# Kernel optimization log

Hardware: AMD Instinct MI355X
Metric: run time of the kernel (lower is better)

## Reference

```python
import jax, jax.numpy as jnp
import numpy as np

B, F, C, H, W = 16, 256, 64, 64, 64   # batch, features, z_channels(e_dim), height, width
N_E = 512                              # codebooksize
BETA = 1.0
EPS = 1e-5


def setup_inputs() -> dict:
    key = jax.random.key(0)
    ks = jax.random.split(key, 4)
    x = jax.random.normal(ks[0], (B, F, H, W), jnp.float32)
    emb = jax.random.normal(ks[1], (N_E, C), jnp.float32)
    emb = emb / jnp.linalg.norm(emb, axis=1, keepdims=True)  # points on hypersphere
    return dict(
        x=x,
        bn1_gamma=jnp.ones((F,), jnp.float32),
        bn1_beta=jnp.zeros((F,), jnp.float32),
        conv1_w=jax.random.normal(ks[2], (C, F), jnp.float32) * np.float32(1.0 / np.sqrt(F)),
        conv1_b=jnp.zeros((C,), jnp.float32),
        conv2_w=jax.random.normal(ks[3], (C, C), jnp.float32) * np.float32(1.0 / np.sqrt(C)),
        conv2_b=jnp.zeros((C,), jnp.float32),
        embedding=emb,
        r=jnp.ones((N_E,), jnp.float32),
    )


def reference(x, bn1_gamma, bn1_beta, conv1_w, conv1_b, conv2_w, conv2_b, embedding, r):
    sg = jax.lax.stop_gradient
    # BatchNorm2d (training mode: batch stats, biased variance)
    mu = x.mean(axis=(0, 2, 3), keepdims=True)
    var = x.var(axis=(0, 2, 3), keepdims=True)
    x1 = (x - mu) * jax.lax.rsqrt(var + EPS)
    x1 = x1 * bn1_gamma[None, :, None, None] + bn1_beta[None, :, None, None]
    # 1x1 convs (note: original overwrites norm2 output, conv2 consumes conv1 output directly)
    x1 = jnp.einsum('bfhw,cf->bchw', x1, conv1_w) + conv1_b[None, :, None, None]
    z = jnp.einsum('bchw,oc->bohw', x1, conv2_w) + conv2_b[None, :, None, None]

    zf = z.reshape(-1, C)  # [B*C*H*W/e_dim view == flat rows of e_dim]
    # codebook angular statistics (norms detached, as torch.Tensor(list) detaches)
    d1 = embedding @ embedding.T                                 # [n_e, n_e]
    en = sg(jnp.linalg.norm(embedding, axis=1))                  # [n_e]
    edx = jnp.clip(d1 / (en[:, None] * en[None, :]), -0.99999, 0.99999)
    ang = jnp.arccos(edx)
    total_min_distance = jnp.mean(jnp.sort(ang, axis=0)[1])      # kthvalue(.,2,dim=0)
    codebookvariance = jnp.mean(jnp.var(ang, axis=1, ddof=1))    # torch.var unbiased

    # VQ dispatch: squared L2 distances + argmin + gather
    d = (zf ** 2).sum(1, keepdims=True) + (embedding ** 2).sum(1) - 2.0 * (zf @ embedding.T)
    idx = jnp.argmin(d, axis=1)                                  # [ntok]
    z_q = embedding[idx].reshape(z.shape)

    hsw = jnp.mean(jnp.square(r - en))
    # legacy=True path with beta=1.0, ignorezq=False, disentangle=True
    loss = jnp.mean((sg(z_q) - z) ** 2) + BETA * jnp.mean((z_q - sg(z)) ** 2)
    loss = loss + hsw + (codebookvariance - total_min_distance)

    z_q = z + sg(z_q - z)  # straight-through
    cb_loss = jnp.float32(0.0)  # prev_cb is None
    r_c = r + sg(jnp.clip(r, 0.9, 1.1) - r)  # Clamp with straight-through grad
    mean_r = jnp.mean(r_c)
    return (loss, z_q, codebookvariance, total_min_distance, hsw, cb_loss, mean_r)
```

## Files before the change

### kernel.cpp

```cpp
#include <hip/hip_runtime.h>
#include <math.h>


#define CAP    2048
#define MARGIN 4e-3f

#define WS_WHI  0
#define WS_WLO  8192
#define WS_BP   16384
#define WS_EN   16448
#define WS_E2   16960
#define WS_ACC  17472
#define WS_CNT  17480
#define WS_WL   17488
#define WS_EFT  19536
#define WS_WD   52304
#define WS_BPD  85072
#define WS_EHI  85200
#define WS_ELO  101584
#define WS_PART 117968
#define WS_SV   122064
#define WS_SM   122576

typedef __attribute__((ext_vector_type(8))) __bf16 bf16v8;
typedef __attribute__((ext_vector_type(2))) __bf16 bf16v2;
typedef __attribute__((ext_vector_type(4))) float  f32v4;
typedef __attribute__((ext_vector_type(4))) unsigned u32v4;

__device__ __forceinline__ unsigned short f2bf(float f) {
    __bf16 h = (__bf16)f;
    return __builtin_bit_cast(unsigned short, h);
}
__device__ __forceinline__ float bf2f(unsigned short h) {
    union { unsigned u; float f; } v; v.u = ((unsigned)h) << 16; return v.f;
}
__device__ __forceinline__ unsigned pack_bf2(float a, float b) {
    bf16v2 v = { (__bf16)a, (__bf16)b };
    return __builtin_bit_cast(unsigned, v);
}
__device__ __forceinline__ float bfhi(float a) {
    return (float)(__bf16)a;
}
__device__ __forceinline__ void load_lds16(const float* g, unsigned* l) {
    __builtin_amdgcn_global_load_lds((const __attribute__((address_space(1))) void*)g,
                                     (__attribute__((address_space(3))) void*)l, 16, 0, 0);
}

__global__ __launch_bounds__(256) void bn_stats_prep(
    const float* __restrict__ x, double* __restrict__ part,
    const float* __restrict__ emb,
    float* __restrict__ eft, float* __restrict__ en, float* __restrict__ e2,
    unsigned short* __restrict__ ehi, unsigned short* __restrict__ elo,
    float* __restrict__ sv, float* __restrict__ sm)
{
    const int t = threadIdx.x;

    if (blockIdx.x < 1024) {
        const int f = blockIdx.x >> 2, ch = blockIdx.x & 3;
        double s0 = 0.0, s1 = 0.0, q0 = 0.0, q1 = 0.0, q2 = 0.0, q3 = 0.0;
        #pragma unroll
        for (int bb = 0; bb < 4; ++bb) {
            const int b = ch * 4 + bb;
            const float4* p = (const float4*)(x + ((size_t)(b * 256 + f) << 12));
            #pragma unroll
            for (int ii = 0; ii < 4; ++ii) {
                float4 u = p[t + ii * 256];
                double dx = u.x, dy = u.y, dz = u.z, dw = u.w;
                s0 += dx + dy; s1 += dz + dw;
                q0 = fma(dx, dx, q0); q1 = fma(dy, dy, q1);
                q2 = fma(dz, dz, q2); q3 = fma(dw, dw, q3);
            }
        }
        double s = s0 + s1, q = (q0 + q1) + (q2 + q3);
        #pragma unroll
        for (int off = 32; off; off >>= 1) { s += __shfl_xor(s, off, 64); q += __shfl_xor(q, off, 64); }
        __shared__ double sh[8];
        const int wv = t >> 6;
        if ((t & 63) == 0) { sh[wv * 2] = s; sh[wv * 2 + 1] = q; }
        __syncthreads();
        if (t == 0) {
            part[blockIdx.x * 2]     = (sh[0] + sh[2]) + (sh[4] + sh[6]);
            part[blockIdx.x * 2 + 1] = (sh[1] + sh[3]) + (sh[5] + sh[7]);
        }
    } else if (blockIdx.x < 1088) {
        const int blk = blockIdx.x - 1024;
        const int lane = t & 63, wv = t >> 6;
        #pragma unroll
        for (int rr = 0; rr < 2; ++rr) {
            int n = blk * 8 + rr * 4 + wv;
            float v = emb[n * 64 + lane];
            eft[lane * 512 + n] = v;
            unsigned short hb = f2bf(v);
            unsigned short lb = f2bf(v - bf2f(hb));
            int pos = (lane >> 3) ^ (n & 7);
            ehi[n * 64 + pos * 8 + (lane & 7)] = hb;
            elo[n * 64 + pos * 8 + (lane & 7)] = lb;
            float qq = v * v;
            #pragma unroll
            for (int off = 32; off; off >>= 1) qq += __shfl_xor(qq, off, 64);
            if (lane == 0) { e2[n] = qq; en[n] = sqrtf(qq); }
        }
    } else {
        const int i = blockIdx.x - 1088;
        const int lane = t & 63, wv = t >> 6;
        __shared__ float ei_sh[64];
        __shared__ float ang[512];
        if (t < 64) ei_sh[t] = emb[(i << 6) + t];
        __syncthreads();
        float ni0 = 0.f, ni1 = 0.f, ni2 = 0.f, ni3 = 0.f;
        #pragma unroll
        for (int k = 0; k < 64; k += 4) {
            ni0 = fmaf(ei_sh[k + 0], ei_sh[k + 0], ni0);
            ni1 = fmaf(ei_sh[k + 1], ei_sh[k + 1], ni1);
            ni2 = fmaf(ei_sh[k + 2], ei_sh[k + 2], ni2);
            ni3 = fmaf(ei_sh[k + 3], ei_sh[k + 3], ni3);
        }
        const float eni = sqrtf((ni0 + ni1) + (ni2 + ni3));
        #pragma unroll
        for (int jj = 0; jj < 2; ++jj) {
            const int j = t + jj * 256;
            const float4* er = (const float4*)(emb + ((size_t)j << 6));
            float d0 = 0.f, d1 = 0.f, d2 = 0.f, d3 = 0.f;
            float n0 = 0.f, n1 = 0.f, n2 = 0.f, n3 = 0.f;
            #pragma unroll
            for (int k4 = 0; k4 < 16; ++k4) {
                float4 u = er[k4];
                const float* e4 = ei_sh + k4 * 4;
                d0 = fmaf(u.x, e4[0], d0); d1 = fmaf(u.y, e4[1], d1);
                d2 = fmaf(u.z, e4[2], d2); d3 = fmaf(u.w, e4[3], d3);
                n0 = fmaf(u.x, u.x, n0);   n1 = fmaf(u.y, u.y, n1);
                n2 = fmaf(u.z, u.z, n2);   n3 = fmaf(u.w, u.w, n3);
            }
            float dot = (d0 + d1) + (d2 + d3);
            float enj = sqrtf((n0 + n1) + (n2 + n3));
            float xv = dot / (eni * enj);
            xv = fminf(fmaxf(xv, -0.99999f), 0.99999f);
            ang[j] = acosf(xv);
        }
        __syncthreads();
        if (wv == 0) {
            float m1 = 3.4e38f, m2 = 3.4e38f, ssum = 0.f;
            #pragma unroll
            for (int t8 = 0; t8 < 8; ++t8) {
                float a = ang[t8 * 64 + lane];
                ssum += a;
                if (a < m1) { m2 = m1; m1 = a; }
                else if (a < m2) m2 = a;
            }
            #pragma unroll
            for (int off = 32; off; off >>= 1) ssum += __shfl_xor(ssum, off, 64);
            #pragma unroll
            for (int off = 32; off; off >>= 1) {
                float o1 = __shfl_xor(m1, off, 64);
                float o2 = __shfl_xor(m2, off, 64);
                if (o1 < m1) { m2 = fminf(m1, o2); m1 = o1; }
                else          m2 = fminf(m2, o1);
            }
            float mean = ssum * (1.f / 512.f);
            float vs = 0.f;
            #pragma unroll
            for (int t8 = 0; t8 < 8; ++t8) {
                float tt = ang[t8 * 64 + lane] - mean;
                vs = fmaf(tt, tt, vs);
            }
            #pragma unroll
            for (int off = 32; off; off >>= 1) vs += __shfl_xor(vs, off, 64);
            if (lane == 0) { sv[i] = vs * (1.f / 511.f); sm[i] = m2; }
        }
    }
}

__global__ __launch_bounds__(256) void prep(
    const float* __restrict__ w1, const float* __restrict__ w2,
    const float* __restrict__ b1, const float* __restrict__ b2,
    const float* __restrict__ gamma, const float* __restrict__ beta,
    const double* __restrict__ part,
    unsigned short* __restrict__ whi, unsigned short* __restrict__ wlo,
    double* __restrict__ Wd,
    double* __restrict__ bpd, float* __restrict__ bp,
    float* __restrict__ accs, int* __restrict__ cnt)
{
    __shared__ double sh_ad[4];
    __shared__ double cdl[256];
    __shared__ double red[4][64];
    __shared__ double tsh[64];
    const int t = threadIdx.x;

    if (blockIdx.x < 64) {
        const int o = t & 63, fi = t >> 6;
        const int f = blockIdx.x * 4 + fi;
        if (o == 0) {
            double s = (part[(4 * f) * 2]     + part[(4 * f + 1) * 2])
                     + (part[(4 * f + 2) * 2] + part[(4 * f + 3) * 2]);
            double q = (part[(4 * f) * 2 + 1]     + part[(4 * f + 1) * 2 + 1])
                     + (part[(4 * f + 2) * 2 + 1] + part[(4 * f + 3) * 2 + 1]);
            double mean = s * (1.0 / 65536.0);
            double var  = q * (1.0 / 65536.0) - mean * mean;
            sh_ad[fi] = (double)gamma[f] / sqrt(var + 1e-5);
        }
        __syncthreads();
        double s = 0.0;
        for (int c = 0; c < 64; ++c)
            s = fma((double)w2[o * 64 + c], (double)w1[c * 256 + f], s);
        double wp = s * sh_ad[fi];
        Wd[o * 256 + f] = wp;
        {
            float wpf = (float)wp;
            unsigned short wh = f2bf(wpf);
            unsigned short wlv = f2bf(wpf - bf2f(wh));
            int mt = o >> 4, cq_ = o & 15, sK = f >> 5, qd_ = (f >> 3) & 3, j = f & 7;
            int idx = ((mt * 8 + sK) * 64 + qd_ * 16 + cq_) * 8 + j;
            whi[idx] = wh; wlo[idx] = wlv;
        }
    } else {
        {
            const int f = t;
            double s = (part[(4 * f) * 2]     + part[(4 * f + 1) * 2])
                     + (part[(4 * f + 2) * 2] + part[(4 * f + 3) * 2]);
            double q = (part[(4 * f) * 2 + 1]     + part[(4 * f + 1) * 2 + 1])
                     + (part[(4 * f + 2) * 2 + 1] + part[(4 * f + 3) * 2 + 1]);
            double mean = s * (1.0 / 65536.0);
            double var  = q * (1.0 / 65536.0) - mean * mean;
            double a = (double)gamma[f] / sqrt(var + 1e-5);
            cdl[f] = (double)beta[f] - mean * a;
        }
        __syncthreads();
        const int o = t & 63, p = t >> 6;
        double ss = 0.0;
        for (int j = 0; j < 64; ++j) {
            int fidx = p * 64 + j;
            ss = fma((double)w1[o * 256 + fidx], cdl[fidx], ss);
        }
        red[p][o] = ss; __syncthreads();
        if (t < 64) tsh[t] = (double)b1[t] + (red[0][t] + red[1][t]) + (red[2][t] + red[3][t]);
        __syncthreads();
        if (t < 64) {
            double bb = (double)b2[t];
            for (int c = 0; c < 64; ++c)
                bb = fma((double)w2[t * 64 + c], tsh[c], bb);
            bpd[t] = bb;
            bp[t]  = (float)bb;
        }
        if (t < 8) accs[t] = 0.f;
        if (t == 0) cnt[0] = 0;
    }
}

__global__ __launch_bounds__(256, 4) void fused_gemm_vq(
    const float* __restrict__ x,
    const unsigned short* __restrict__ whi,
    const unsigned short* __restrict__ wlo,
    const float* __restrict__ bp,
    const float* __restrict__ emb,
    const float* __restrict__ e2,
    const unsigned short* __restrict__ ehi,
    const unsigned short* __restrict__ elo,
    float* __restrict__ accs,
    int* __restrict__ cnt, int* __restrict__ wl,
    float* __restrict__ zq)
{
    __shared__ __align__(16) unsigned smem[4880];
    enum { OAR = 0,
           OE2 = 4096, OZ2 = 4608, ODT = 4672, OD2T = 4736, OIT = 4800 };
    float* e2s = (float*)(smem + OE2);
    float* z2s = (float*)(smem + OZ2);
    float* dT  = (float*)(smem + ODT);
    float* d2T = (float*)(smem + OD2T);
    int*   iT  = (int*)(smem + OIT);

    const int tid = threadIdx.x, lane = tid & 63, wv = tid >> 6;
    const int wvu = __builtin_amdgcn_readfirstlane(wv);
    const int lb = ((blockIdx.x & 7) << 7) | (blockIdx.x >> 3);
    const int b = lb >> 6, h = lb & 63;
    const int cq = lane & 15, qd = lane >> 4;

    bf16v8 Ahi[8], Alo[8];
    #pragma unroll
    for (int s = 0; s < 8; ++s) {
        Ahi[s] = *(const bf16v8*)(whi + ((size_t)((wvu * 8 + s) * 64 + lane)) * 8);
        Alo[s] = *(const bf16v8*)(wlo + ((size_t)((wvu * 8 + s) * 64 + lane)) * 8);
    }
    float bpv[4];
    #pragma unroll
    for (int r = 0; r < 4; ++r) bpv[r] = bp[wvu * 16 + qd * 4 + r];
    e2s[tid]       = e2[tid];
    e2s[tid + 256] = e2[tid + 256];

    const float* xb = x + ((size_t)(b * 256 + wvu * 16) << 12) + (h << 6) + lane;
    float xva[16], xvb[16];
    #pragma unroll
    for (int i = 0; i < 16; ++i) xva[i] = xb[(size_t)i << 12];
    #pragma unroll
    for (int i = 0; i < 16; ++i) xvb[i] = xb[((size_t)(64 + i)) << 12];

    f32v4 acc[4];
    #pragma unroll
    for (int nt = 0; nt < 4; ++nt) acc[nt] = (f32v4){bpv[0], bpv[1], bpv[2], bpv[3]};

#define GEMM_CHUNK(CHK, CUR)                                                          \
    {                                                                                 \
        __syncthreads();                                                 \
        {                                                                             \
            unsigned hb[8], lbv[8];                                                   \
            _Pragma("unroll")                                                         \
            for (int p = 0; p < 8; ++p) {                                             \
                float a = CUR[2 * p], bq = CUR[2 * p + 1];                            \
                hb[p] = pack_bf2(a, bq);                                              \
                lbv[p] = pack_bf2(a - bfhi(a), bq - bfhi(bq));                        \
            }                                                                         \
            const int b0 = lane * 32 + (((2 * wvu) ^ (lane & 7)) << 2);               \
            const int b1 = lane * 32 + (((2 * wvu + 1) ^ (lane & 7)) << 2);           \
            *(u32v4*)(smem + OAR + b0)        = (u32v4){hb[0], hb[1], hb[2], hb[3]};  \
            *(u32v4*)(smem + OAR + b1)        = (u32v4){hb[4], hb[5], hb[6], hb[7]};  \
            *(u32v4*)(smem + OAR + 2048 + b0) = (u32v4){lbv[0], lbv[1], lbv[2], lbv[3]}; \
            *(u32v4*)(smem + OAR + 2048 + b1) = (u32v4){lbv[4], lbv[5], lbv[6], lbv[7]}; \
        }                                                                             \
        __syncthreads();                                                \
        if (CHK < 2) {                               \
            const float* xb2 = xb + ((size_t)((CHK + 2) * 64) << 12);                 \
            _Pragma("unroll")                                                         \
            for (int i = 0; i < 16; ++i) CUR[i] = xb2[(size_t)i << 12];               \
        }                                                                             \
        _Pragma("unroll")                                                             \
        for (int st2 = 0; st2 < 2; ++st2) {                                           \
            const int s = CHK * 2 + st2;                                              \
            _Pragma("unroll")                                                         \
            for (int nt = 0; nt < 4; ++nt) {                                          \
                const int row = nt * 16 + cq;                                         \
                const int pos = row * 32 + (((st2 * 4 + qd) ^ (row & 7)) << 2);       \
                bf16v8 bh = *(const bf16v8*)(smem + OAR + pos);                       \
                bf16v8 bl = *(const bf16v8*)(smem + OAR + 2048 + pos);                \
                acc[nt] = __builtin_amdgcn_mfma_f32_16x16x32_bf16(Ahi[s], bh, acc[nt], 0, 0, 0); \
                acc[nt] = __builtin_amdgcn_mfma_f32_16x16x32_bf16(Ahi[s], bl, acc[nt], 0, 0, 0); \
                acc[nt] = __builtin_amdgcn_mfma_f32_16x16x32_bf16(Alo[s], bh, acc[nt], 0, 0, 0); \
            }                                                                         \
        }                                                                             \
    }

    GEMM_CHUNK(0, xva)
    GEMM_CHUNK(1, xvb)
    GEMM_CHUNK(2, xva)
    GEMM_CHUNK(3, xvb)
#undef GEMM_CHUNK

    __syncthreads();

    {
        float z2p[4];
        #pragma unroll
        for (int r = 0; r < 4; ++r) {
            float p2 = 0.f;
            #pragma unroll
            for (int nt = 0; nt < 4; ++nt) p2 = fmaf(acc[nt][r], acc[nt][r], p2);
            #pragma unroll
            for (int off = 1; off <= 8; off <<= 1) p2 += __shfl_xor(p2, off, 64);
            z2p[r] = p2;
        }
        if (cq == 0) {
            #pragma unroll
            for (int r = 0; r < 4; ++r) z2s[wvu * 16 + qd * 4 + r] = z2p[r];
        }
        unsigned short* ar = (unsigned short*)(smem + OAR);
        #pragma unroll
        for (int nt = 0; nt < 4; ++nt) {
            const int w = nt * 16 + cq;
            const int gz = w >> 3, kj = w & 7;
            #pragma unroll
            for (int r = 0; r < 4; ++r) {
                const int tok = wvu * 16 + qd * 4 + r;
                const int hw = tok * 64 + ((gz ^ (tok & 7)) << 3) + kj;
                unsigned short zh = f2bf(acc[nt][r]);
                ar[hw]        = zh;
                ar[4096 + hw] = f2bf(acc[nt][r] - bf2f(zh));
            }
        }
    }
    __syncthreads();

    const int x7 = cq & 7;
    bf16v8 vahi[2], valo[2];
    {
        const int rbase = (wvu * 16 + cq) * 32;
        #pragma unroll
        for (int s = 0; s < 2; ++s) {
            int pos = ((s * 4 + qd) ^ x7) * 4;
            vahi[s] = *(const bf16v8*)(smem + OAR + rbase + pos);
            valo[s] = *(const bf16v8*)(smem + OAR + 2048 + rbase + pos);
        }
    }
    __syncthreads();

    {
        const float* gh = (const float*)ehi;
        const float* gl = (const float*)elo;
        load_lds16(gh + wvu * 256 + lane * 4,        smem + OAR + wvu * 256);
        load_lds16(gl + wvu * 256 + lane * 4,        smem + OAR + 1024 + wvu * 256);
        load_lds16(gh + 1024 + wvu * 256 + lane * 4, smem + OAR + 2048 + wvu * 256);
        load_lds16(gl + 1024 + wvu * 256 + lane * 4, smem + OAR + 3072 + wvu * 256);
    }

    float m1[4] = {-3.4e38f, -3.4e38f, -3.4e38f, -3.4e38f};
    float m2[4] = {-3.4e38f, -3.4e38f, -3.4e38f, -3.4e38f};
    int   i1[4] = {0, 0, 0, 0};
    const int p0 = (qd ^ x7) * 4, p1 = ((4 + qd) ^ x7) * 4;

    #pragma unroll 1
    for (int t2 = 0; t2 < 32; ++t2) {
        if ((t2 & 1) == 0) {
            __syncthreads();
            int st = t2 >> 1;
            if (st >= 1 && st < 15) {
                const float* gh = (const float*)ehi + (size_t)(st + 1) * 1024;
                const float* gl = (const float*)elo + (size_t)(st + 1) * 1024;
                unsigned* dst = smem + OAR + ((st + 1) & 1) * 2048;
                load_lds16(gh + wvu * 256 + lane * 4, dst + wvu * 256);
                load_lds16(gl + wvu * 256 + lane * 4, dst + 1024 + wvu * 256);
            }
        }
        const int rb = OAR + ((t2 >> 1) & 1) * 2048 + ((t2 & 1) * 16 + cq) * 32;
        bf16v8 bh0 = *(const bf16v8*)(smem + rb + p0);
        bf16v8 bh1 = *(const bf16v8*)(smem + rb + p1);
        bf16v8 bl0 = *(const bf16v8*)(smem + rb + 1024 + p0);
        bf16v8 bl1 = *(const bf16v8*)(smem + rb + 1024 + p1);
        const float eps = e2s[t2 * 16 + cq];
        f32v4 a = {0.f, 0.f, 0.f, 0.f};
        __builtin_amdgcn_s_setprio(1);
        a = __builtin_amdgcn_mfma_f32_16x16x32_bf16(vahi[0], bh0, a, 0, 0, 0);
        a = __builtin_amdgcn_mfma_f32_16x16x32_bf16(vahi[1], bh1, a, 0, 0, 0);
        a = __builtin_amdgcn_mfma_f32_16x16x32_bf16(vahi[0], bl0, a, 0, 0, 0);
        a = __builtin_amdgcn_mfma_f32_16x16x32_bf16(vahi[1], bl1, a, 0, 0, 0);
        a = __builtin_amdgcn_mfma_f32_16x16x32_bf16(valo[0], bh0, a, 0, 0, 0);
        a = __builtin_amdgcn_mfma_f32_16x16x32_bf16(valo[1], bh1, a, 0, 0, 0);
        __builtin_amdgcn_s_setprio(0);
        const int n = t2 * 16 + cq;
        #pragma unroll
        for (int r = 0; r < 4; ++r) {
            float s = fmaf(-0.5f, eps, a[r]);
            bool gt = s > m1[r];
            m2[r] = fminf(fmaxf(s, m2[r]), m1[r]);
            i1[r] = gt ? n : i1[r];
            m1[r] = fmaxf(s, m1[r]);
        }
    }

    #pragma unroll
    for (int r = 0; r < 4; ++r) {
        #pragma unroll
        for (int off = 1; off <= 8; off <<= 1) {
            float o1 = __shfl_xor(m1[r], off, 64);
            float o2 = __shfl_xor(m2[r], off, 64);
            int   oi = __shfl_xor(i1[r], off, 64);
            if (o1 > m1[r] || (o1 == m1[r] && oi < i1[r])) {
                m2[r] = fmaxf(m1[r], o2); m1[r] = o1; i1[r] = oi;
            } else {
                m2[r] = fmaxf(m2[r], o1);
            }
        }
    }
    if (cq == 0) {
        #pragma unroll
        for (int r = 0; r < 4; ++r) {
            int tok = wvu * 16 + qd * 4 + r;
            dT[tok] = m1[r]; d2T[tok] = m2[r]; iT[tok] = i1[r];
        }
    }
    __syncthreads();

    if (wv == 0) {
        float s1 = dT[lane], s2 = d2T[lane];
        if (s1 - s2 < MARGIN * 0.5f) {
            int pos = atomicAdd(cnt, 1);
            if (pos < CAP) wl[pos] = ((b << 6) + lane) * 64 + h;
        }
        float ms = z2s[lane] - 2.f * s1;
        #pragma unroll
        for (int off = 32; off; off >>= 1) ms += __shfl_xor(ms, off, 64);
        if (lane == 0) atomicAdd(accs + 0, ms);
    }
    __syncthreads();

    float* zrow = zq + ((size_t)(b * 64) << 12) + (h << 6) + lane;
    #pragma unroll
    for (int cc = 0; cc < 16; ++cc) {
        int c = wvu * 16 + cc;
        int id = iT[c];
        zrow[(size_t)c << 12] = emb[(id << 6) + lane];
    }
}

__global__ __launch_bounds__(256) void refine_fin(
    const float* __restrict__ x,
    const double* __restrict__ Wd,
    const double* __restrict__ bpd,
    const float* __restrict__ emb,
    const float* __restrict__ eft,
    const int* __restrict__ cnt, const int* __restrict__ wl,
    float* __restrict__ zq,
    const float* __restrict__ accs, const float* __restrict__ en,
    const float* __restrict__ sv, const float* __restrict__ sm,
    const float* __restrict__ r, float* __restrict__ out)
{
    const int tid = threadIdx.x, lane = tid & 63, wv = tid >> 6;

    if (blockIdx.x == 2048) {
        if (wv == 0) {
            float hs = 0.f, rs = 0.f, cv = 0.f, tm = 0.f;
            #pragma unroll
            for (int jj = 0; jj < 8; ++jj) {
                int n = (jj << 6) + lane;
                float rv = r[n];
                float d = rv - en[n];
                hs = fmaf(d, d, hs);
                rs += fminf(fmaxf(rv, 0.9f), 1.1f);
                cv += sv[n];
                tm += sm[n];
            }
            #pragma unroll
            for (int off = 32; off; off >>= 1) {
                hs += __shfl_xor(hs, off, 64); rs += __shfl_xor(rs, off, 64);
                cv += __shfl_xor(cv, off, 64); tm += __shfl_xor(tm, off, 64);
            }
            if (lane == 0) {
                float hsw    = hs * (1.f / 512.f);
                float mean_r = rs * (1.f / 512.f);
                float mse    = accs[0] * (1.f / 4194304.f);
                float cbv    = cv * (1.f / 512.f);
                float tmd    = tm * (1.f / 512.f);
                float loss   = 2.f * mse + hsw + (cbv - tmd);
                out[0]       = loss;
                out[4194305] = cbv;
                out[4194306] = tmd;
                out[4194307] = hsw;
                out[4194308] = 0.f;
                out[4194309] = mean_r;
            }
        }
        return;
    }

    int count = cnt[0]; if (count > CAP) count = CAP;
    const int it = blockIdx.x;
    if (it >= count) return;

    __shared__ double zp[4][64];
    __shared__ double zs[64];
    __shared__ double dsh[4];
    __shared__ int    ish[4];

    const int r2 = wl[it];
    const int b = r2 >> 12, c = (r2 >> 6) & 63, h = r2 & 63;

    {
        const float* xp = x + (((size_t)(b * 256 + wv * 64)) << 12) + (h << 6) + lane;
        const double* wrow = Wd + c * 256 + wv * 64;
        double zc0 = 0.0, zc1 = 0.0, zc2 = 0.0, zc3 = 0.0;
        double zc4 = 0.0, zc5 = 0.0, zc6 = 0.0, zc7 = 0.0;
        #pragma unroll
        for (int f = 0; f < 64; f += 8) {
            float a0 = xp[(size_t)(f + 0) << 12];
            float a1 = xp[(size_t)(f + 1) << 12];
            float a2 = xp[(size_t)(f + 2) << 12];
            float a3 = xp[(size_t)(f + 3) << 12];
            float a4 = xp[(size_t)(f + 4) << 12];
            float a5 = xp[(size_t)(f + 5) << 12];
            float a6 = xp[(size_t)(f + 6) << 12];
            float a7 = xp[(size_t)(f + 7) << 12];
            zc0 = fma(wrow[f + 0], (double)a0, zc0);
            zc1 = fma(wrow[f + 1], (double)a1, zc1);
            zc2 = fma(wrow[f + 2], (double)a2, zc2);
            zc3 = fma(wrow[f + 3], (double)a3, zc3);
            zc4 = fma(wrow[f + 4], (double)a4, zc4);
            zc5 = fma(wrow[f + 5], (double)a5, zc5);
            zc6 = fma(wrow[f + 6], (double)a6, zc6);
            zc7 = fma(wrow[f + 7], (double)a7, zc7);
        }
        zp[wv][lane] = ((zc0 + zc1) + (zc2 + zc3)) + ((zc4 + zc5) + (zc6 + zc7));
    }
    __syncthreads();
    if (tid < 64) zs[tid] = (zp[0][tid] + zp[1][tid]) + (zp[2][tid] + zp[3][tid]) + bpd[c];
    __syncthreads();

    const int n0 = tid, n1 = tid + 256;
    double d0a = 0.0, d0b = 0.0, d0c = 0.0, d0d = 0.0;
    double d1a = 0.0, d1b = 0.0, d1c = 0.0, d1d = 0.0;
    #pragma unroll 4
    for (int k = 0; k < 64; k += 4) {
        double z0 = zs[k], z1 = zs[k + 1], z2 = zs[k + 2], z3 = zs[k + 3];
        double t;
        t = z0 - (double)eft[((k + 0) << 9) + n0]; d0a = fma(t, t, d0a);
        t = z1 - (double)eft[((k + 1) << 9) + n0]; d0b = fma(t, t, d0b);
        t = z2 - (double)eft[((k + 2) << 9) + n0]; d0c = fma(t, t, d0c);
        t = z3 - (double)eft[((k + 3) << 9) + n0]; d0d = fma(t, t, d0d);
        t = z0 - (double)eft[((k + 0) << 9) + n1]; d1a = fma(t, t, d1a);
        t = z1 - (double)eft[((k + 1) << 9) + n1]; d1b = fma(t, t, d1b);
        t = z2 - (double)eft[((k + 2) << 9) + n1]; d1c = fma(t, t, d1c);
        t = z3 - (double)eft[((k + 3) << 9) + n1]; d1d = fma(t, t, d1d);
    }
    double d0 = (d0a + d0b) + (d0c + d0d);
    double d1 = (d1a + d1b) + (d1c + d1d);
    double dm; int im;
    if (d1 < d0) { dm = d1; im = n1; } else { dm = d0; im = n0; }

    #pragma unroll
    for (int off = 32; off; off >>= 1) {
        double od = __shfl_xor(dm, off, 64);
        int    oi = __shfl_xor(im, off, 64);
        if (od < dm || (od == dm && oi < im)) { dm = od; im = oi; }
    }
    if (lane == 0) { dsh[wv] = dm; ish[wv] = im; }
    __syncthreads();

    if (tid < 64) {
        double best = dsh[0]; int bi = ish[0];
        #pragma unroll
        for (int wq = 1; wq < 4; ++wq) {
            double od = dsh[wq]; int oi = ish[wq];
            if (od < best || (od == best && oi < bi)) { best = od; bi = oi; }
        }
        zq[((size_t)r2 << 6) + tid] = emb[(bi << 6) + tid];
    }
}

extern "C" void kernel_launch(void* const* d_in, const int* in_sizes, int n_in,
                              void* d_out, int out_size, void* d_ws, size_t ws_size,
                              hipStream_t stream) {
    const float* x   = (const float*)d_in[0];
    const float* g1  = (const float*)d_in[1];
    const float* be1 = (const float*)d_in[2];
    const float* w1  = (const float*)d_in[3];
    const float* b1  = (const float*)d_in[4];
    const float* w2  = (const float*)d_in[5];
    const float* b2  = (const float*)d_in[6];
    const float* emb = (const float*)d_in[7];
    const float* r   = (const float*)d_in[8];
    float* ws = (float*)d_ws;
    float* out = (float*)d_out;

    double* WD   = (double*)(ws + WS_WD);
    double* BPD  = (double*)(ws + WS_BPD);
    double* PART = (double*)(ws + WS_PART);
    int*    CNT  = (int*)(ws + WS_CNT);
    int*    WL   = (int*)(ws + WS_WL);
    unsigned short* WHI = (unsigned short*)(ws + WS_WHI);
    unsigned short* WLO = (unsigned short*)(ws + WS_WLO);
    unsigned short* EHI = (unsigned short*)(ws + WS_EHI);
    unsigned short* ELO = (unsigned short*)(ws + WS_ELO);

    bn_stats_prep<<<1600, 256, 0, stream>>>(x, PART, emb,
                                            ws + WS_EFT, ws + WS_EN, ws + WS_E2,
                                            EHI, ELO, ws + WS_SV, ws + WS_SM);
    prep<<<65, 256, 0, stream>>>(w1, w2, b1, b2, g1, be1, PART,
                                 WHI, WLO, WD, BPD, ws + WS_BP,
                                 ws + WS_ACC, CNT);
    fused_gemm_vq<<<1024, 256, 0, stream>>>(x, WHI, WLO, ws + WS_BP,
                                            emb, ws + WS_E2,
                                            EHI, ELO, ws + WS_ACC, CNT, WL, out + 1);
    refine_fin<<<2049, 256, 0, stream>>>(x, WD, BPD, emb, ws + WS_EFT, CNT, WL,
                                         out + 1, ws + WS_ACC, ws + WS_EN,
                                         ws + WS_SV, ws + WS_SM, r, out);
}
```

Baseline: 181.7 us.

## Eliminate prep kernel by folding BN scale into GEMM consumers

Removes the separate prep launch. The unscaled W2·W1 product and its bf16 hi/lo split are now computed inside the stats kernel, which does not depend on x. Each fused_gemm_vq block recomputes the BN scale/shift and folded bias from the partial sums, then applies the per-feature scale to x before the bf16 split. refine_fin likewise recomputes scale and bias per block, and accumulator zeroing moves to a memset. This saves one launch and its serialization, at the cost of redundant per-block prologue work (256-way reductions and 64x64 double dot products) in 1024 and 2049 blocks. The hi/lo bf16 split now covers the unscaled weights and separately the scaled activations, which shifts rounding error.

Measured after the change: 190.7 us. 4.9% more time.

```diff
diff --git a/kernel.cpp b/kernel.cpp
--- a/kernel.cpp
+++ b/kernel.cpp
@@ -7,7 +7,6 @@
 
 #define WS_WHI  0
 #define WS_WLO  8192
-#define WS_BP   16384
 #define WS_EN   16448
 #define WS_E2   16960
 #define WS_ACC  17472
@@ -15,7 +14,6 @@
 #define WS_WL   17488
 #define WS_EFT  19536
 #define WS_WD   52304
-#define WS_BPD  85072
 #define WS_EHI  85200
 #define WS_ELO  101584
 #define WS_PART 117968
@@ -46,44 +44,87 @@
                                      (__attribute__((address_space(3))) void*)l, 16, 0, 0);
 }
 
-__global__ __launch_bounds__(256) void bn_stats_prep(
+__global__ __launch_bounds__(256) void bn_stats_fold(
     const float* __restrict__ x, double* __restrict__ part,
     const float* __restrict__ emb,
+    const float* __restrict__ w1, const float* __restrict__ w2,
     float* __restrict__ eft, float* __restrict__ en, float* __restrict__ e2,
     unsigned short* __restrict__ ehi, unsigned short* __restrict__ elo,
-    float* __restrict__ sv, float* __restrict__ sm)
+    float* __restrict__ sv, float* __restrict__ sm,
+    double* __restrict__ Ud,
+    unsigned short* __restrict__ whi, unsigned short* __restrict__ wlo)
 {
     const int t = threadIdx.x;
 
-    if (blockIdx.x < 1024) {
-        const int f = blockIdx.x >> 2, ch = blockIdx.x & 3;
-        double s0 = 0.0, s1 = 0.0, q0 = 0.0, q1 = 0.0, q2 = 0.0, q3 = 0.0;
-        #pragma unroll
-        for (int bb = 0; bb < 4; ++bb) {
-            const int b = ch * 4 + bb;
-            const float4* p = (const float4*)(x + ((size_t)(b * 256 + f) << 12));
-            #pragma unroll
-            for (int ii = 0; ii < 4; ++ii) {
-                float4 u = p[t + ii * 256];
-                double dx = u.x, dy = u.y, dz = u.z, dw = u.w;
-                s0 += dx + dy; s1 += dz + dw;
-                q0 = fma(dx, dx, q0); q1 = fma(dy, dy, q1);
-                q2 = fma(dz, dz, q2); q3 = fma(dw, dw, q3);
-            }
-        }
-        double s = s0 + s1, q = (q0 + q1) + (q2 + q3);
-        #pragma unroll
-        for (int off = 32; off; off >>= 1) { s += __shfl_xor(s, off, 64); q += __shfl_xor(q, off, 64); }
-        __shared__ double sh[8];
-        const int wv = t >> 6;
-        if ((t & 63) == 0) { sh[wv * 2] = s; sh[wv * 2 + 1] = q; }
+    if (blockIdx.x < 512) {
+        const int i = blockIdx.x;
+        const int lane = t & 63, wv = t >> 6;
+        __shared__ float ei_sh[64];
+        __shared__ float ang[512];
+        if (t < 64) ei_sh[t] = emb[(i << 6) + t];
         __syncthreads();
-        if (t == 0) {
-            part[blockIdx.x * 2]     = (sh[0] + sh[2]) + (sh[4] + sh[6]);
-            part[blockIdx.x * 2 + 1] = (sh[1] + sh[3]) + (sh[5] + sh[7]);
-        }
-    } else if (blockIdx.x < 1088) {
-        const int blk = blockIdx.x - 1024;
+        float ni0 = 0.f, ni1 = 0.f, ni2 = 0.f, ni3 = 0.f;
+        #pragma unroll
+        for (int k = 0; k < 64; k += 4) {
+            ni0 = fmaf(ei_sh[k + 0], ei_sh[k + 0], ni0);
+            ni1 = fmaf(ei_sh[k + 1], ei_sh[k + 1], ni1);
+            ni2 = fmaf(ei_sh[k + 2], ei_sh[k + 2], ni2);
+            ni3 = fmaf(ei_sh[k + 3], ei_sh[k + 3], ni3);
+        }
+        const float eni = sqrtf((ni0 + ni1) + (ni2 + ni3));
+        #pragma unroll
+        for (int jj = 0; jj < 2; ++jj) {
+            const int j = t + jj * 256;
+            const float4* er = (const float4*)(emb + ((size_t)j << 6));
+            float d0 = 0.f, d1 = 0.f, d2 = 0.f, d3 = 0.f;
+            float n0 = 0.f, n1 = 0.f, n2 = 0.f, n3 = 0.f;
+            #pragma unroll
+            for (int k4 = 0; k4 < 16; ++k4) {
+                float4 u = er[k4];
+                const float* e4 = ei_sh + k4 * 4;
+                d0 = fmaf(u.x, e4[0], d0); d1 = fmaf(u.y, e4[1], d1);
+                d2 = fmaf(u.z, e4[2], d2); d3 = fmaf(u.w, e4[3], d3);
+                n0 = fmaf(u.x, u.x, n0);   n1 = fmaf(u.y, u.y, n1);
+                n2 = fmaf(u.z, u.z, n2);   n3 = fmaf(u.w, u.w, n3);
+            }
+            float dot = (d0 + d1) + (d2 + d3);
+            float enj = sqrtf((n0 + n1) + (n2 + n3));
+            float xv = dot / (eni * enj);
+            xv = fminf(fmaxf(xv, -0.99999f), 0.99999f);
+            ang[j] = acosf(xv);
+        }
+        __syncthreads();
+        if (wv == 0) {
+            float m1 = 3.4e38f, m2 = 3.4e38f, ssum = 0.f;
+            #pragma unroll
+            for (int t8 = 0; t8 < 8; ++t8) {
+                float a = ang[t8 * 64 + lane];
+                ssum += a;
+                if (a < m1) { m2 = m1; m1 = a; }
+                else if (a < m2) m2 = a;
+            }
+            #pragma unroll
+            for (int off = 32; off; off >>= 1) ssum += __shfl_xor(ssum, off, 64);
+            #pragma unroll
+            for (int off = 32; off; off >>= 1) {
+                float o1 = __shfl_xor(m1, off, 64);
+                float o2 = __shfl_xor(m2, off, 64);
+                if (o1 < m1) { m2 = fminf(m1, o2); m1 = o1; }
+                else          m2 = fminf(m2, o1);
+            }
+            float mean = ssum * (1.f / 512.f);
+            float vs = 0.f;
+            #pragma unroll
+            for (int t8 = 0; t8 < 8; ++t8) {
+                float tt = ang[t8 * 64 + lane] - mean;
+                vs = fmaf(tt, tt, vs);
+            }
+            #pragma unroll
+            for (int off = 32; off; off >>= 1) vs += __shfl_xor(vs, off, 64);
+            if (lane == 0) { sv[i] = vs * (1.f / 511.f); sm[i] = m2; }
+        }
+    } else if (blockIdx.x < 576) {
+        const int blk = blockIdx.x - 512;
         const int lane = t & 63, wv = t >> 6;
         #pragma unroll
         for (int rr = 0; rr < 2; ++rr) {
@@ -100,149 +141,48 @@
             for (int off = 32; off; off >>= 1) qq += __shfl_xor(qq, off, 64);
             if (lane == 0) { e2[n] = qq; en[n] = sqrtf(qq); }
         }
-    } else {
-        const int i = blockIdx.x - 1088;
-        const int lane = t & 63, wv = t >> 6;
-        __shared__ float ei_sh[64];
-        __shared__ float ang[512];
-        if (t < 64) ei_sh[t] = emb[(i << 6) + t];
-        __syncthreads();
-        float ni0 = 0.f, ni1 = 0.f, ni2 = 0.f, ni3 = 0.f;
-        #pragma unroll
-        for (int k = 0; k < 64; k += 4) {
-            ni0 = fmaf(ei_sh[k + 0], ei_sh[k + 0], ni0);
-            ni1 = fmaf(ei_sh[k + 1], ei_sh[k + 1], ni1);
-            ni2 = fmaf(ei_sh[k + 2], ei_sh[k + 2], ni2);
-            ni3 = fmaf(ei_sh[k + 3], ei_sh[k + 3], ni3);
-        }
-        const float eni = sqrtf((ni0 + ni1) + (ni2 + ni3));
-        #pragma unroll
-        for (int jj = 0; jj < 2; ++jj) {
-            const int j = t + jj * 256;
-            const float4* er = (const float4*)(emb + ((size_t)j << 6));
-            float d0 = 0.f, d1 = 0.f, d2 = 0.f, d3 = 0.f;
-            float n0 = 0.f, n1 = 0.f, n2 = 0.f, n3 = 0.f;
-            #pragma unroll
-            for (int k4 = 0; k4 < 16; ++k4) {
-                float4 u = er[k4];
-                const float* e4 = ei_sh + k4 * 4;
-                d0 = fmaf(u.x, e4[0], d0); d1 = fmaf(u.y, e4[1], d1);
-                d2 = fmaf(u.z, e4[2], d2); d3 = fmaf(u.w, e4[3], d3);
-                n0 = fmaf(u.x, u.x, n0);   n1 = fmaf(u.y, u.y, n1);
-                n2 = fmaf(u.z, u.z, n2);   n3 = fmaf(u.w, u.w, n3);
-            }
-            float dot = (d0 + d1) + (d2 + d3);
-            float enj = sqrtf((n0 + n1) + (n2 + n3));
-            float xv = dot / (eni * enj);
-            xv = fminf(fmaxf(xv, -0.99999f), 0.99999f);
-            ang[j] = acosf(xv);
-        }
-        __syncthreads();
-        if (wv == 0) {
-            float m1 = 3.4e38f, m2 = 3.4e38f, ssum = 0.f;
-            #pragma unroll
-            for (int t8 = 0; t8 < 8; ++t8) {
-                float a = ang[t8 * 64 + lane];
-                ssum += a;
-                if (a < m1) { m2 = m1; m1 = a; }
-                else if (a < m2) m2 = a;
-            }
-            #pragma unroll
-            for (int off = 32; off; off >>= 1) ssum += __shfl_xor(ssum, off, 64);
-            #pragma unroll
-            for (int off = 32; off; off >>= 1) {
-                float o1 = __shfl_xor(m1, off, 64);
-                float o2 = __shfl_xor(m2, off, 64);
-                if (o1 < m1) { m2 = fminf(m1, o2); m1 = o1; }
-                else          m2 = fminf(m2, o1);
-            }
-            float mean = ssum * (1.f / 512.f);
-            float vs = 0.f;
-            #pragma unroll
-            for (int t8 = 0; t8 < 8; ++t8) {
-                float tt = ang[t8 * 64 + lane] - mean;
-                vs = fmaf(tt, tt, vs);
-            }
-            #pragma unroll
-            for (int off = 32; off; off >>= 1) vs += __shfl_xor(vs, off, 64);
-            if (lane == 0) { sv[i] = vs * (1.f / 511.f); sm[i] = m2; }
-        }
-    }
-}
-
-__global__ __launch_bounds__(256) void prep(
-    const float* __restrict__ w1, const float* __restrict__ w2,
-    const float* __restrict__ b1, const float* __restrict__ b2,
-    const float* __restrict__ gamma, const float* __restrict__ beta,
-    const double* __restrict__ part,
-    unsigned short* __restrict__ whi, unsigned short* __restrict__ wlo,
-    double* __restrict__ Wd,
-    double* __restrict__ bpd, float* __restrict__ bp,
-    float* __restrict__ accs, int* __restrict__ cnt)
-{
-    __shared__ double sh_ad[4];
-    __shared__ double cdl[256];
-    __shared__ double red[4][64];
-    __shared__ double tsh[64];
-    const int t = threadIdx.x;
-
-    if (blockIdx.x < 64) {
+    } else if (blockIdx.x < 640) {
+        const int blk = blockIdx.x - 576;
         const int o = t & 63, fi = t >> 6;
-        const int f = blockIdx.x * 4 + fi;
-        if (o == 0) {
-            double s = (part[(4 * f) * 2]     + part[(4 * f + 1) * 2])
-                     + (part[(4 * f + 2) * 2] + part[(4 * f + 3) * 2]);
-            double q = (part[(4 * f) * 2 + 1]     + part[(4 * f + 1) * 2 + 1])
-                     + (part[(4 * f + 2) * 2 + 1] + part[(4 * f + 3) * 2 + 1]);
-            double mean = s * (1.0 / 65536.0);
-            double var  = q * (1.0 / 65536.0) - mean * mean;
-            sh_ad[fi] = (double)gamma[f] / sqrt(var + 1e-5);
-        }
-        __syncthreads();
+        const int f = blk * 4 + fi;
         double s = 0.0;
         for (int c = 0; c < 64; ++c)
             s = fma((double)w2[o * 64 + c], (double)w1[c * 256 + f], s);
-        double wp = s * sh_ad[fi];
-        Wd[o * 256 + f] = wp;
-        {
-            float wpf = (float)wp;
-            unsigned short wh = f2bf(wpf);
-            unsigned short wlv = f2bf(wpf - bf2f(wh));
-            int mt = o >> 4, cq_ = o & 15, sK = f >> 5, qd_ = (f >> 3) & 3, j = f & 7;
-            int idx = ((mt * 8 + sK) * 64 + qd_ * 16 + cq_) * 8 + j;
-            whi[idx] = wh; wlo[idx] = wlv;
-        }
+        Ud[o * 256 + f] = s;
+        float wpf = (float)s;
+        unsigned short wh = f2bf(wpf);
+        unsigned short wlv = f2bf(wpf - bf2f(wh));
+        int mt = o >> 4, cq_ = o & 15, sK = f >> 5, qd_ = (f >> 3) & 3, j = f & 7;
+        int idx = ((mt * 8 + sK) * 64 + qd_ * 16 + cq_) * 8 + j;
+        whi[idx] = wh; wlo[idx] = wlv;
     } else {
-        {
-            const int f = t;
-            double s = (part[(4 * f) * 2]     + part[(4 * f + 1) * 2])
-                     + (part[(4 * f + 2) * 2] + part[(4 * f + 3) * 2]);
-            double q = (part[(4 * f) * 2 + 1]     + part[(4 * f + 1) * 2 + 1])
-                     + (part[(4 * f + 2) * 2 + 1] + part[(4 * f + 3) * 2 + 1]);
-            double mean = s * (1.0 / 65536.0);
-            double var  = q * (1.0 / 65536.0) - mean * mean;
-            double a = (double)gamma[f] / sqrt(var + 1e-5);
-            cdl[f] = (double)beta[f] - mean * a;
-        }
+        const int idx = blockIdx.x - 640;
+        const int f = idx >> 2, ch = idx & 3;
+        double s0 = 0.0, s1 = 0.0, q0 = 0.0, q1 = 0.0, q2 = 0.0, q3 = 0.0;
+        #pragma unroll
+        for (int bb = 0; bb < 4; ++bb) {
+            const int b = ch * 4 + bb;
+            const float4* p = (const float4*)(x + ((size_t)(b * 256 + f) << 12));
+            #pragma unroll
+            for (int ii = 0; ii < 4; ++ii) {
+                float4 u = p[t + ii * 256];
+                double dx = u.x, dy = u.y, dz = u.z, dw = u.w;
+                s0 += dx + dy; s1 += dz + dw;
+                q0 = fma(dx, dx, q0); q1 = fma(dy, dy, q1);
+                q2 = fma(dz, dz, q2); q3 = fma(dw, dw, q3);
+            }
+        }
+        double s = s0 + s1, q = (q0 + q1) + (q2 + q3);
+        #pragma unroll
+        for (int off = 32; off; off >>= 1) { s += __shfl_xor(s, off, 64); q += __shfl_xor(q, off, 64); }
+        __shared__ double sh[8];
+        const int wv = t >> 6;
+        if ((t & 63) == 0) { sh[wv * 2] = s; sh[wv * 2 + 1] = q; }
         __syncthreads();
-        const int o = t & 63, p = t >> 6;
-        double ss = 0.0;
-        for (int j = 0; j < 64; ++j) {
-            int fidx = p * 64 + j;
-            ss = fma((double)w1[o * 256 + fidx], cdl[fidx], ss);
-        }
-        red[p][o] = ss; __syncthreads();
-        if (t < 64) tsh[t] = (double)b1[t] + (red[0][t] + red[1][t]) + (red[2][t] + red[3][t]);
-        __syncthreads();
-        if (t < 64) {
-            double bb = (double)b2[t];
-            for (int c = 0; c < 64; ++c)
-                bb = fma((double)w2[t * 64 + c], tsh[c], bb);
-            bpd[t] = bb;
-            bp[t]  = (float)bb;
-        }
-        if (t < 8) accs[t] = 0.f;
-        if (t == 0) cnt[0] = 0;
+        if (t == 0) {
+            part[idx * 2]     = (sh[0] + sh[2]) + (sh[4] + sh[6]);
+            part[idx * 2 + 1] = (sh[1] + sh[3]) + (sh[5] + sh[7]);
+        }
     }
 }
 
@@ -250,7 +190,10 @@
     const float* __restrict__ x,
     const unsigned short* __restrict__ whi,
     const unsigned short* __restrict__ wlo,
-    const float* __restrict__ bp,
+    const double* __restrict__ part,
+    const float* __restrict__ gamma, const float* __restrict__ beta,
+    const float* __restrict__ w1, const float* __restrict__ b1,
+    const float* __restrict__ w2, const float* __restrict__ b2,
     const float* __restrict__ emb,
     const float* __restrict__ e2,
     const unsigned short* __restrict__ ehi,
@@ -274,17 +217,54 @@
     const int b = lb >> 6, h = lb & 63;
     const int cq = lane & 15, qd = lane >> 4;
 
+    float bpv[4];
+    {
+        double* cdl  = (double*)(smem + OAR);
+        double* red  = (double*)(smem + OAR + 512);
+        double* tshd = (double*)(smem + OAR + 1024);
+        float*  bpf  = (float*)(smem + OAR + 1152);
+        float*  af_s = (float*)(smem + OE2);
+        {
+            const int f = tid;
+            double s = (part[(4 * f) * 2]     + part[(4 * f + 1) * 2])
+                     + (part[(4 * f + 2) * 2] + part[(4 * f + 3) * 2]);
+            double q = (part[(4 * f) * 2 + 1]     + part[(4 * f + 1) * 2 + 1])
+                     + (part[(4 * f + 2) * 2 + 1] + part[(4 * f + 3) * 2 + 1]);
+            double mean = s * (1.0 / 65536.0);
+            double var  = q * (1.0 / 65536.0) - mean * mean;
+            double a = (double)gamma[f] / sqrt(var + 1e-5);
+            af_s[f] = (float)a;
+            cdl[f]  = (double)beta[f] - mean * a;
+        }
+        __syncthreads();
+        {
+            const int o = tid & 63, p = tid >> 6;
+            double ss = 0.0;
+            for (int j = 0; j < 64; ++j)
+                ss = fma((double)w1[o * 256 + p * 64 + j], cdl[p * 64 + j], ss);
+            red[p * 64 + o] = ss;
+        }
+        __syncthreads();
+        if (tid < 64) tshd[tid] = (double)b1[tid] + (red[tid] + red[64 + tid]) + (red[128 + tid] + red[192 + tid]);
+        __syncthreads();
+        if (tid < 64) {
+            double bb = (double)b2[tid];
+            for (int k = 0; k < 64; ++k)
+                bb = fma((double)w2[tid * 64 + k], tshd[k], bb);
+            bpf[tid] = (float)bb;
+        }
+        __syncthreads();
+        #pragma unroll
+        for (int r = 0; r < 4; ++r) bpv[r] = bpf[wvu * 16 + qd * 4 + r];
+    }
+    const float* af_s = (const float*)(smem + OE2);
+
     bf16v8 Ahi[8], Alo[8];
     #pragma unroll
     for (int s = 0; s < 8; ++s) {
         Ahi[s] = *(const bf16v8*)(whi + ((size_t)((wvu * 8 + s) * 64 + lane)) * 8);
         Alo[s] = *(const bf16v8*)(wlo + ((size_t)((wvu * 8 + s) * 64 + lane)) * 8);
     }
-    float bpv[4];
-    #pragma unroll
-    for (int r = 0; r < 4; ++r) bpv[r] = bp[wvu * 16 + qd * 4 + r];
-    e2s[tid]       = e2[tid];
-    e2s[tid + 256] = e2[tid + 256];
 
     const float* xb = x + ((size_t)(b * 256 + wvu * 16) << 12) + (h << 6) + lane;
     float xva[16], xvb[16];
@@ -299,21 +279,25 @@
 
 #define GEMM_CHUNK(CHK, CUR)                                                          \
     {                                                                                 \
+        float afv[16];                                                                \
+        _Pragma("unroll")                                                             \
+        for (int i = 0; i < 16; ++i) afv[i] = af_s[CHK * 64 + wvu * 16 + i];          \
         __syncthreads();                                                 \
         {                                                                             \
             unsigned hb[8], lbv[8];                                                   \
             _Pragma("unroll")                                                         \
             for (int p = 0; p < 8; ++p) {                                             \
-                float a = CUR[2 * p], bq = CUR[2 * p + 1];                            \
+                float a = afv[2 * p] * CUR[2 * p];                                    \
+                float bq = afv[2 * p + 1] * CUR[2 * p + 1];                           \
                 hb[p] = pack_bf2(a, bq);                                              \
                 lbv[p] = pack_bf2(a - bfhi(a), bq - bfhi(bq));                        \
             }                                                                         \
             const int b0 = lane * 32 + (((2 * wvu) ^ (lane & 7)) << 2);               \
-            const int b1 = lane * 32 + (((2 * wvu + 1) ^ (lane & 7)) << 2);           \
-            *(u32v4*)(smem + OAR + b0)        = (u32v4){hb[0], hb[1], hb[2], hb[3]};  \
-            *(u32v4*)(smem + OAR + b1)        = (u32v4){hb[4], hb[5], hb[6], hb[7]};  \
-            *(u32v4*)(smem + OAR + 2048 + b0) = (u32v4){lbv[0], lbv[1], lbv[2], lbv[3]}; \
-            *(u32v4*)(smem + OAR + 2048 + b1) = (u32v4){lbv[4], lbv[5], lbv[6], lbv[7]}; \
+            const int b1_ = lane * 32 + (((2 * wvu + 1) ^ (lane & 7)) << 2);          \
+            *(u32v4*)(smem + OAR + b0)         = (u32v4){hb[0], hb[1], hb[2], hb[3]}; \
+            *(u32v4*)(smem + OAR + b1_)        = (u32v4){hb[4], hb[5], hb[6], hb[7]}; \
+            *(u32v4*)(smem + OAR + 2048 + b0)  = (u32v4){lbv[0], lbv[1], lbv[2], lbv[3]}; \
+            *(u32v4*)(smem + OAR + 2048 + b1_) = (u32v4){lbv[4], lbv[5], lbv[6], lbv[7]}; \
         }                                                                             \
         __syncthreads();                                                \
         if (CHK < 2) {                               \
@@ -345,6 +329,9 @@
 
     __syncthreads();
 
+    e2s[tid]       = e2[tid];
+    e2s[tid + 256] = e2[tid + 256];
+
     {
         float z2p[4];
         #pragma unroll
@@ -490,8 +477,11 @@
 
 __global__ __launch_bounds__(256) void refine_fin(
     const float* __restrict__ x,
-    const double* __restrict__ Wd,
-    const double* __restrict__ bpd,
+    const double* __restrict__ Ud,
+    const double* __restrict__ part,
+    const float* __restrict__ gamma, const float* __restrict__ beta,
+    const float* __restrict__ b1, const float* __restrict__ b2,
+    const float* __restrict__ w2,
     const float* __restrict__ emb,
     const float* __restrict__ eft,
     const int* __restrict__ cnt, const int* __restrict__ wl,
@@ -546,13 +536,36 @@
     __shared__ double zs[64];
     __shared__ double dsh[4];
     __shared__ int    ish[4];
+    __shared__ double adl[256];
+    __shared__ double bsh;
 
     const int r2 = wl[it];
     const int b = r2 >> 12, c = (r2 >> 6) & 63, h = r2 & 63;
 
     {
+        const int f = tid;
+        double s = (part[(4 * f) * 2]     + part[(4 * f + 1) * 2])
+                 + (part[(4 * f + 2) * 2] + part[(4 * f + 3) * 2]);
+        double q = (part[(4 * f) * 2 + 1]     + part[(4 * f + 1) * 2 + 1])
+                 + (part[(4 * f + 2) * 2 + 1] + part[(4 * f + 3) * 2 + 1]);
+        double mean = s * (1.0 / 65536.0);
+        double var  = q * (1.0 / 65536.0) - mean * mean;
+        double a = (double)gamma[f] / sqrt(var + 1e-5);
+        adl[f] = a;
+        double cdlv = (double)beta[f] - mean * a;
+        double p = Ud[c * 256 + f] * cdlv;
+        if (tid < 64) p = fma((double)w2[c * 64 + tid], (double)b1[tid], p);
+        #pragma unroll
+        for (int off = 32; off; off >>= 1) p += __shfl_xor(p, off, 64);
+        if (lane == 0) dsh[wv] = p;
+    }
+    __syncthreads();
+    if (tid == 0) bsh = (double)b2[c] + (dsh[0] + dsh[1]) + (dsh[2] + dsh[3]);
+
+    {
         const float* xp = x + (((size_t)(b * 256 + wv * 64)) << 12) + (h << 6) + lane;
-        const double* wrow = Wd + c * 256 + wv * 64;
+        const double* urow = Ud + c * 256 + wv * 64;
+        const double* arow = adl + wv * 64;
         double zc0 = 0.0, zc1 = 0.0, zc2 = 0.0, zc3 = 0.0;
         double zc4 = 0.0, zc5 = 0.0, zc6 = 0.0, zc7 = 0.0;
         #pragma unroll
@@ -565,19 +578,19 @@
             float a5 = xp[(size_t)(f + 5) << 12];
             float a6 = xp[(size_t)(f + 6) << 12];
             float a7 = xp[(size_t)(f + 7) << 12];
-            zc0 = fma(wrow[f + 0], (double)a0, zc0);
-            zc1 = fma(wrow[f + 1], (double)a1, zc1);
-            zc2 = fma(wrow[f + 2], (double)a2, zc2);
-            zc3 = fma(wrow[f + 3], (double)a3, zc3);
-            zc4 = fma(wrow[f + 4], (double)a4, zc4);
-            zc5 = fma(wrow[f + 5], (double)a5, zc5);
-            zc6 = fma(wrow[f + 6], (double)a6, zc6);
-            zc7 = fma(wrow[f + 7], (double)a7, zc7);
+            zc0 = fma(urow[f + 0] * arow[f + 0], (double)a0, zc0);
+            zc1 = fma(urow[f + 1] * arow[f + 1], (double)a1, zc1);
+            zc2 = fma(urow[f + 2] * arow[f + 2], (double)a2, zc2);
+            zc3 = fma(urow[f + 3] * arow[f + 3], (double)a3, zc3);
+            zc4 = fma(urow[f + 4] * arow[f + 4], (double)a4, zc4);
+            zc5 = fma(urow[f + 5] * arow[f + 5], (double)a5, zc5);
+            zc6 = fma(urow[f + 6] * arow[f + 6], (double)a6, zc6);
+            zc7 = fma(urow[f + 7] * arow[f + 7], (double)a7, zc7);
         }
         zp[wv][lane] = ((zc0 + zc1) + (zc2 + zc3)) + ((zc4 + zc5) + (zc6 + zc7));
     }
     __syncthreads();
-    if (tid < 64) zs[tid] = (zp[0][tid] + zp[1][tid]) + (zp[2][tid] + zp[3][tid]) + bpd[c];
+    if (tid < 64) zs[tid] = (zp[0][tid] + zp[1][tid]) + (zp[2][tid] + zp[3][tid]) + bsh;
     __syncthreads();
 
     const int n0 = tid, n1 = tid + 256;
@@ -636,8 +649,7 @@
     float* ws = (float*)d_ws;
     float* out = (float*)d_out;
 
-    double* WD   = (double*)(ws + WS_WD);
-    double* BPD  = (double*)(ws + WS_BPD);
+    double* UD   = (double*)(ws + WS_WD);
     double* PART = (double*)(ws + WS_PART);
     int*    CNT  = (int*)(ws + WS_CNT);
     int*    WL   = (int*)(ws + WS_WL);
@@ -646,16 +658,18 @@
     unsigned short* EHI = (unsigned short*)(ws + WS_EHI);
     unsigned short* ELO = (unsigned short*)(ws + WS_ELO);
 
-    bn_stats_prep<<<1600, 256, 0, stream>>>(x, PART, emb,
+    hipMemsetAsync(ws + WS_ACC, 0, 64, stream);
+
+    bn_stats_fold<<<1664, 256, 0, stream>>>(x, PART, emb, w1, w2,
                                             ws + WS_EFT, ws + WS_EN, ws + WS_E2,
-                                            EHI, ELO, ws + WS_SV, ws + WS_SM);
-    prep<<<65, 256, 0, stream>>>(w1, w2, b1, b2, g1, be1, PART,
-                                 WHI, WLO, WD, BPD, ws + WS_BP,
-                                 ws + WS_ACC, CNT);
-    fused_gemm_vq<<<1024, 256, 0, stream>>>(x, WHI, WLO, ws + WS_BP,
+                                            EHI, ELO, ws + WS_SV, ws + WS_SM,
+                                            UD, WHI, WLO);
+    fused_gemm_vq<<<1024, 256, 0, stream>>>(x, WHI, WLO, PART, g1, be1,
+                                            w1, b1, w2, b2,
                                             emb, ws + WS_E2,
                                             EHI, ELO, ws + WS_ACC, CNT, WL, out + 1);
-    refine_fin<<<2049, 256, 0, stream>>>(x, WD, BPD, emb, ws + WS_EFT, CNT, WL,
+    refine_fin<<<2049, 256, 0, stream>>>(x, UD, PART, g1, be1, b1, b2, w2,
+                                         emb, ws + WS_EFT, CNT, WL,
                                          out + 1, ws + WS_ACC, ws + WS_EN,
                                          ws + WS_SV, ws + WS_SM, r, out);
 }
```

## Fold prep kernel into stats kernel using atomic ticket spin-wait

Applied to the files above, without the earlier changes.

Merges the separate prep launch into bn_stats_prep as 65 extra blocks. These blocks spin on an atomic ticket counter until all 1024 BN-statistics blocks have published their partial sums. The aim is to drop one kernel launch and its inter-kernel gap. It adds a hipMemsetAsync to reset the counter, and the spin-wait relies on the waiting blocks being scheduled after, or alongside, the producer blocks, so it risks deadlock or wasted CU time if they are not.

After: 220.1 us. 1.21x slower.

```diff
diff --git a/kernel.cpp b/kernel.cpp
--- a/kernel.cpp
+++ b/kernel.cpp
@@ -21,6 +21,7 @@
 #define WS_PART 117968
 #define WS_SV   122064
 #define WS_SM   122576
+#define WS_TKT  123088
 
 typedef __attribute__((ext_vector_type(8))) __bf16 bf16v8;
 typedef __attribute__((ext_vector_type(2))) __bf16 bf16v2;
@@ -49,9 +50,15 @@
 __global__ __launch_bounds__(256) void bn_stats_prep(
     const float* __restrict__ x, double* __restrict__ part,
     const float* __restrict__ emb,
+    const float* __restrict__ w1, const float* __restrict__ w2,
+    const float* __restrict__ b1, const float* __restrict__ b2,
+    const float* __restrict__ gamma, const float* __restrict__ beta,
     float* __restrict__ eft, float* __restrict__ en, float* __restrict__ e2,
     unsigned short* __restrict__ ehi, unsigned short* __restrict__ elo,
-    float* __restrict__ sv, float* __restrict__ sm)
+    float* __restrict__ sv, float* __restrict__ sm,
+    unsigned short* __restrict__ whi, unsigned short* __restrict__ wlo,
+    double* __restrict__ Wd, double* __restrict__ bpd, float* __restrict__ bp,
+    float* __restrict__ accs, int* __restrict__ cnt, int* __restrict__ tkt)
 {
     const int t = threadIdx.x;
 
@@ -81,6 +88,8 @@
         if (t == 0) {
             part[blockIdx.x * 2]     = (sh[0] + sh[2]) + (sh[4] + sh[6]);
             part[blockIdx.x * 2 + 1] = (sh[1] + sh[3]) + (sh[5] + sh[7]);
+            __threadfence();
+            atomicAdd(tkt, 1);
         }
     } else if (blockIdx.x < 1088) {
         const int blk = blockIdx.x - 1024;
@@ -100,7 +109,7 @@
             for (int off = 32; off; off >>= 1) qq += __shfl_xor(qq, off, 64);
             if (lane == 0) { e2[n] = qq; en[n] = sqrtf(qq); }
         }
-    } else {
+    } else if (blockIdx.x < 1600) {
         const int i = blockIdx.x - 1088;
         const int lane = t & 63, wv = t >> 6;
         __shared__ float ei_sh[64];
@@ -167,28 +176,16 @@
             for (int off = 32; off; off >>= 1) vs += __shfl_xor(vs, off, 64);
             if (lane == 0) { sv[i] = vs * (1.f / 511.f); sm[i] = m2; }
         }
-    }
-}
-
-__global__ __launch_bounds__(256) void prep(
-    const float* __restrict__ w1, const float* __restrict__ w2,
-    const float* __restrict__ b1, const float* __restrict__ b2,
-    const float* __restrict__ gamma, const float* __restrict__ beta,
-    const double* __restrict__ part,
-    unsigned short* __restrict__ whi, unsigned short* __restrict__ wlo,
-    double* __restrict__ Wd,
-    double* __restrict__ bpd, float* __restrict__ bp,
-    float* __restrict__ accs, int* __restrict__ cnt)
-{
-    __shared__ double sh_ad[4];
-    __shared__ double cdl[256];
-    __shared__ double red[4][64];
-    __shared__ double tsh[64];
-    const int t = threadIdx.x;
-
-    if (blockIdx.x < 64) {
+    } else if (blockIdx.x < 1664) {
+        if (t == 0) {
+            while (__hip_atomic_load(tkt, __ATOMIC_ACQUIRE, __HIP_MEMORY_SCOPE_AGENT) < 1024)
+                __builtin_amdgcn_s_sleep(8);
+        }
+        __syncthreads();
+        __shared__ double sh_ad[4];
+        const int blk = blockIdx.x - 1600;
         const int o = t & 63, fi = t >> 6;
-        const int f = blockIdx.x * 4 + fi;
+        const int f = blk * 4 + fi;
         if (o == 0) {
             double s = (part[(4 * f) * 2]     + part[(4 * f + 1) * 2])
                      + (part[(4 * f + 2) * 2] + part[(4 * f + 3) * 2]);
@@ -204,15 +201,21 @@
             s = fma((double)w2[o * 64 + c], (double)w1[c * 256 + f], s);
         double wp = s * sh_ad[fi];
         Wd[o * 256 + f] = wp;
-        {
-            float wpf = (float)wp;
-            unsigned short wh = f2bf(wpf);
-            unsigned short wlv = f2bf(wpf - bf2f(wh));
-            int mt = o >> 4, cq_ = o & 15, sK = f >> 5, qd_ = (f >> 3) & 3, j = f & 7;
-            int idx = ((mt * 8 + sK) * 64 + qd_ * 16 + cq_) * 8 + j;
-            whi[idx] = wh; wlo[idx] = wlv;
-        }
+        float wpf = (float)wp;
+        unsigned short wh = f2bf(wpf);
+        unsigned short wlv = f2bf(wpf - bf2f(wh));
+        int mt = o >> 4, cq_ = o & 15, sK = f >> 5, qd_ = (f >> 3) & 3, j = f & 7;
+        int idx = ((mt * 8 + sK) * 64 + qd_ * 16 + cq_) * 8 + j;
+        whi[idx] = wh; wlo[idx] = wlv;
     } else {
+        if (t == 0) {
+            while (__hip_atomic_load(tkt, __ATOMIC_ACQUIRE, __HIP_MEMORY_SCOPE_AGENT) < 1024)
+                __builtin_amdgcn_s_sleep(8);
+        }
+        __syncthreads();
+        __shared__ double cdl[256];
+        __shared__ double red[4][64];
+        __shared__ double tsh[64];
         {
             const int f = t;
             double s = (part[(4 * f) * 2]     + part[(4 * f + 1) * 2])
@@ -309,11 +312,11 @@
                 lbv[p] = pack_bf2(a - bfhi(a), bq - bfhi(bq));                        \
             }                                                                         \
             const int b0 = lane * 32 + (((2 * wvu) ^ (lane & 7)) << 2);               \
-            const int b1 = lane * 32 + (((2 * wvu + 1) ^ (lane & 7)) << 2);           \
-            *(u32v4*)(smem + OAR + b0)        = (u32v4){hb[0], hb[1], hb[2], hb[3]};  \
-            *(u32v4*)(smem + OAR + b1)        = (u32v4){hb[4], hb[5], hb[6], hb[7]};  \
-            *(u32v4*)(smem + OAR + 2048 + b0) = (u32v4){lbv[0], lbv[1], lbv[2], lbv[3]}; \
-            *(u32v4*)(smem + OAR + 2048 + b1) = (u32v4){lbv[4], lbv[5], lbv[6], lbv[7]}; \
+            const int b1_ = lane * 32 + (((2 * wvu + 1) ^ (lane & 7)) << 2);          \
+            *(u32v4*)(smem + OAR + b0)         = (u32v4){hb[0], hb[1], hb[2], hb[3]}; \
+            *(u32v4*)(smem + OAR + b1_)        = (u32v4){hb[4], hb[5], hb[6], hb[7]}; \
+            *(u32v4*)(smem + OAR + 2048 + b0)  = (u32v4){lbv[0], lbv[1], lbv[2], lbv[3]}; \
+            *(u32v4*)(smem + OAR + 2048 + b1_) = (u32v4){lbv[4], lbv[5], lbv[6], lbv[7]}; \
         }                                                                             \
         __syncthreads();                                                \
         if (CHK < 2) {                               \
@@ -641,17 +644,18 @@
     double* PART = (double*)(ws + WS_PART);
     int*    CNT  = (int*)(ws + WS_CNT);
     int*    WL   = (int*)(ws + WS_WL);
+    int*    TKT  = (int*)(ws + WS_TKT);
     unsigned short* WHI = (unsigned short*)(ws + WS_WHI);
     unsigned short* WLO = (unsigned short*)(ws + WS_WLO);
     unsigned short* EHI = (unsigned short*)(ws + WS_EHI);
     unsigned short* ELO = (unsigned short*)(ws + WS_ELO);
 
-    bn_stats_prep<<<1600, 256, 0, stream>>>(x, PART, emb,
+    hipMemsetAsync(TKT, 0, 4, stream);
+    bn_stats_prep<<<1665, 256, 0, stream>>>(x, PART, emb, w1, w2, b1, b2, g1, be1,
                                             ws + WS_EFT, ws + WS_EN, ws + WS_E2,
-                                            EHI, ELO, ws + WS_SV, ws + WS_SM);
-    prep<<<65, 256, 0, stream>>>(w1, w2, b1, b2, g1, be1, PART,
-                                 WHI, WLO, WD, BPD, ws + WS_BP,
-                                 ws + WS_ACC, CNT);
+                                            EHI, ELO, ws + WS_SV, ws + WS_SM,
+                                            WHI, WLO, WD, BPD, ws + WS_BP,
+                                            ws + WS_ACC, CNT, TKT);
     fused_gemm_vq<<<1024, 256, 0, stream>>>(x, WHI, WLO, ws + WS_BP,
                                             emb, ws + WS_E2,
                                             EHI, ELO, ws + WS_ACC, CNT, WL, out + 1);
```
